# Performance work log

Measured on AMD Instinct MI355X. Metric: run time of the kernel, lower is better.

Reference implementation:

```python
import jax, jax.numpy as jnp
import numpy as np

MODES = 16
DIM = 16      # comb(modes + photons - 1, photons) with photons=1 -> modes
BATCH = 32768


def _mesh_targets(modes):
    # Full rectangular Clements mesh, 0-indexed mode pairs, modes*(modes-1)/2 elements.
    pairs = []
    for layer in range(modes):
        for i in range(layer % 2, modes - 1, 2):
            pairs.append((i, i + 1))
    return np.asarray(pairs, dtype=np.int32)


def setup_inputs() -> dict:
    key = jax.random.key(0)
    k1, k2, k3 = jax.random.split(key, 3)
    targets = jnp.asarray(_mesh_targets(MODES))  # [120, 2] int32
    E = targets.shape[0]
    params = jax.random.normal(k1, (BATCH, 2 * E), dtype=jnp.float32)
    state_re = jax.random.normal(k2, (BATCH, DIM, DIM), dtype=jnp.float32)
    state_im = jax.random.normal(k3, (BATCH, DIM, DIM), dtype=jnp.float32)
    return {"params": params, "state_re": state_re, "state_im": state_im, "targets": targets}


def _clements_unitary(theta, phi, m_idx, n_idx):
    # Sequentially embed 2x2 MZI blocks T(m,n,theta,phi) into a DIMxDIM unitary:
    # U <- T @ U, where T is identity except rows (m, n):
    #   T[m,m]=e^{i phi} cos th, T[m,n]=-sin th, T[n,m]=e^{i phi} sin th, T[n,n]=cos th
    # Only two rows of U change per step, so we update rows instead of a full matmul.
    U0 = jnp.eye(DIM, dtype=jnp.complex64)

    def step(U, x):
        mi, ni, t, p = x
        c = jnp.cos(t)
        s = jnp.sin(t)
        e = jnp.exp(1j * p)  # complex64
        rm = U[mi]
        rn = U[ni]
        U = U.at[mi].set(e * c * rm - s * rn)
        U = U.at[ni].set(e * s * rm + c * rn)
        return U, None

    U, _ = jax.lax.scan(step, U0, (m_idx, n_idx, theta, phi))
    # diag phases are all zero in UParamLayer.map_clements -> identity, skipped.
    return U


def reference(params, state_re, state_im, targets):
    E = targets.shape[0]
    theta = params[:, :E]          # [B, E]
    phi = params[:, E:2 * E]       # [B, E]
    m_idx = targets[:, 0]
    n_idx = targets[:, 1]

    U = jax.vmap(lambda t, p: _clements_unitary(t, p, m_idx, n_idx))(theta, phi)  # [B, D, D] c64
    rho = jax.lax.complex(state_re, state_im)  # [B, D, D] c64

    left = jnp.einsum('bij,bjk->bik', U, rho)             # U @ rho
    out = jnp.einsum('bik,bjk->bij', left, jnp.conj(U))   # (U @ rho) @ U^dagger
    # Return real/imag stacked so the baseline output is a plain float tensor.
    return jnp.stack([out.real, out.imag], axis=1)  # [B, 2, D, D] f32
```

## Files before the change

kernel.cpp:

```cpp
#include <hip/hip_runtime.h>

#define DIM 16
#define NE 120
#define ITEMS 8
#define THREADS 128
#define UITEM 1032
#define LDS_FLOATS (ITEMS * UITEM)

typedef float v2f __attribute__((ext_vector_type(2)));


__global__ __launch_bounds__(THREADS, 2) void uparam_kernel(
    const float* __restrict__ params,
    const float* __restrict__ state_re,
    const float* __restrict__ state_im,
    float* __restrict__ out)
{
    __shared__ float lds[LDS_FLOATS];

    const int tid  = threadIdx.x;
    const int item = tid >> 4;
    const int c    = tid & 15;
    const long b   = (long)blockIdx.x * ITEMS + item;

    float* slot = lds + item * UITEM;
    float* aux  = slot + 512;

    {
        const float* prow = params + b * (2 * NE);
        #pragma unroll
        for (int k = 0; k < 15; ++k) {
            const int a = k * 16 + c;
            float sv, cv;
            __sincosf(prow[a], &sv, &cv);
            const int e   = (a < NE) ? a : a - NE;
            const int off = (a < NE) ? 0 : 2;
            *(float2*)(aux + 4 * e + off) = make_float2(cv, sv);
        }
    }

    const float* rre = state_re + b * (DIM * DIM);
    const float* rim = state_im + b * (DIM * DIM);
    float prr[16], pri[16];
    #pragma unroll
    for (int k = 0; k < 16; ++k) { prr[k] = rre[k * 16 + c]; pri[k] = rim[k * 16 + c]; }

    asm volatile("s_waitcnt lgkmcnt(0)" ::: "memory");

    v2f Uv[DIM];
    #pragma unroll
    for (int i = 0; i < DIM; ++i) Uv[i] = (v2f){ (i == c) ? 1.0f : 0.0f, 0.0f };

    #pragma unroll 1
    for (int l2 = 0; l2 < 8; ++l2) {
        const int eb = l2 * 15;
        #pragma unroll
        for (int j = 0; j < 15; ++j) {
            const int m = (j < 8) ? 2 * j : 2 * (j - 8) + 1;
            const int n = m + 1;
            const float4 cs = *(const float4*)(aux + 4 * (eb + j));
            const float ct = cs.x, st = cs.y, cp = cs.z, sp = cs.w;
            const v2f um = Uv[m], un = Uv[n];
            const v2f jm = { -um.y, um.x };
            const v2f w  = cp * um + sp * jm;
            Uv[m] = ct * w - st * un;
            Uv[n] = st * w + ct * un;
        }
    }

    #pragma unroll
    for (int q = 0; q < 8; ++q) {
        const int qq = q ^ (c & 7);
        *(float4*)(slot + c * 32 + qq * 4) =
            make_float4(Uv[2*q].x, Uv[2*q].y, Uv[2*q+1].x, Uv[2*q+1].y);
    }

    asm volatile("s_waitcnt lgkmcnt(0)" ::: "memory");

    v2f L[DIM];
    #pragma unroll
    for (int i = 0; i < DIM; ++i) L[i] = (v2f)(0.0f);

    #pragma unroll
    for (int k = 0; k < 16; ++k) {
        const float* ucol = slot + k * 32;
        const int kx = k & 7;
        const float4 q0 = *(const float4*)(ucol + (0 ^ kx) * 4);
        const float4 q1 = *(const float4*)(ucol + (1 ^ kx) * 4);
        const float4 q2 = *(const float4*)(ucol + (2 ^ kx) * 4);
        const float4 q3 = *(const float4*)(ucol + (3 ^ kx) * 4);
        const float4 q4 = *(const float4*)(ucol + (4 ^ kx) * 4);
        const float4 q5 = *(const float4*)(ucol + (5 ^ kx) * 4);
        const float4 q6 = *(const float4*)(ucol + (6 ^ kx) * 4);
        const float4 q7 = *(const float4*)(ucol + (7 ^ kx) * 4);
        const float pr = prr[k], pi = pri[k];
        v2f u[16];
        u[0]=(v2f){q0.x,q0.y}; u[1]=(v2f){q0.z,q0.w}; u[2]=(v2f){q1.x,q1.y}; u[3]=(v2f){q1.z,q1.w};
        u[4]=(v2f){q2.x,q2.y}; u[5]=(v2f){q2.z,q2.w}; u[6]=(v2f){q3.x,q3.y}; u[7]=(v2f){q3.z,q3.w};
        u[8]=(v2f){q4.x,q4.y}; u[9]=(v2f){q4.z,q4.w}; u[10]=(v2f){q5.x,q5.y}; u[11]=(v2f){q5.z,q5.w};
        u[12]=(v2f){q6.x,q6.y}; u[13]=(v2f){q6.z,q6.w}; u[14]=(v2f){q7.x,q7.y}; u[15]=(v2f){q7.z,q7.w};
        #pragma unroll
        for (int i = 0; i < 16; ++i) {
            L[i] += u[i] * pr;
            L[i] += (v2f){ -u[i].y, u[i].x } * pi;
        }
    }

    #pragma unroll
    for (int i = 0; i < 16; ++i)
        *(v2f*)(aux + i * 32 + 2 * (c ^ i)) = L[i];

    asm volatile("s_waitcnt lgkmcnt(0)" ::: "memory");

    v2f acc[DIM];
    #pragma unroll
    for (int j = 0; j < DIM; ++j) acc[j] = (v2f)(0.0f);

    #pragma unroll 4
    for (int k = 0; k < 16; ++k) {
        const v2f lk = *(const v2f*)(aux + c * 32 + 2 * (k ^ c));
        const float* ucol = slot + k * 32;
        const int kx = k & 7;
        const float4 q0 = *(const float4*)(ucol + (0 ^ kx) * 4);
        const float4 q1 = *(const float4*)(ucol + (1 ^ kx) * 4);
        const float4 q2 = *(const float4*)(ucol + (2 ^ kx) * 4);
        const float4 q3 = *(const float4*)(ucol + (3 ^ kx) * 4);
        const float4 q4 = *(const float4*)(ucol + (4 ^ kx) * 4);
        const float4 q5 = *(const float4*)(ucol + (5 ^ kx) * 4);
        const float4 q6 = *(const float4*)(ucol + (6 ^ kx) * 4);
        const float4 q7 = *(const float4*)(ucol + (7 ^ kx) * 4);
        v2f u[16];
        u[0]=(v2f){q0.x,q0.y}; u[1]=(v2f){q0.z,q0.w}; u[2]=(v2f){q1.x,q1.y}; u[3]=(v2f){q1.z,q1.w};
        u[4]=(v2f){q2.x,q2.y}; u[5]=(v2f){q2.z,q2.w}; u[6]=(v2f){q3.x,q3.y}; u[7]=(v2f){q3.z,q3.w};
        u[8]=(v2f){q4.x,q4.y}; u[9]=(v2f){q4.z,q4.w}; u[10]=(v2f){q5.x,q5.y}; u[11]=(v2f){q5.z,q5.w};
        u[12]=(v2f){q6.x,q6.y}; u[13]=(v2f){q6.z,q6.w}; u[14]=(v2f){q7.x,q7.y}; u[15]=(v2f){q7.z,q7.w};
        const float lr = lk.x, li = lk.y;
        #pragma unroll
        for (int j = 0; j < 16; ++j) {
            acc[j] += u[j] * lr;
            acc[j] += (v2f){ u[j].y, -u[j].x } * li;
        }
    }

    float* outp = out + b * (2 * DIM * DIM) + c * DIM;
    #pragma unroll
    for (int q = 0; q < 4; ++q) {
        *(float4*)(outp + 4 * q) =
            make_float4(acc[4*q].x, acc[4*q+1].x, acc[4*q+2].x, acc[4*q+3].x);
        *(float4*)(outp + DIM * DIM + 4 * q) =
            make_float4(-acc[4*q].y, -acc[4*q+1].y, -acc[4*q+2].y, -acc[4*q+3].y);
    }
}

extern "C" void kernel_launch(void* const* d_in, const int* in_sizes, int n_in,
                              void* d_out, int out_size, void* d_ws, size_t ws_size,
                              hipStream_t stream) {
    const float* params   = (const float*)d_in[0];
    const float* state_re = (const float*)d_in[1];
    const float* state_im = (const float*)d_in[2];
    float* out = (float*)d_out;

    const int batch = in_sizes[0] / (2 * NE);
    dim3 grid(batch / ITEMS);
    uparam_kernel<<<grid, THREADS, 0, stream>>>(params, state_re, state_im, out);
}
```

Baseline: 69.87 us.

## Shrink blocks to one wave, stage angles in two halves, transpose via shuffles

The block shrinks from two waves and 8 batch items to one wave and 4 items. The angle table in LDS is halved by computing sincos and building the MZI update for 60 elements at a time in two passes, with the raw angles held in registers. The LDS round trip that transposed L is replaced by a butterfly of __shfl_xor exchanges. Together these cut LDS per item and LDS traffic, which should raise occupancy. The costs are extra shuffle instructions, and L[k] is indexed inside a loop that is only unrolled by 4, so the compiler may spill L to scratch.

```diff
diff --git a/kernel.cpp b/kernel.cpp
--- a/kernel.cpp
+++ b/kernel.cpp
@@ -2,9 +2,9 @@
 
 #define DIM 16
 #define NE 120
-#define ITEMS 8
-#define THREADS 128
-#define UITEM 1032
+#define ITEMS 4
+#define THREADS 64
+#define UITEM 760
 #define LDS_FLOATS (ITEMS * UITEM)
 
 typedef float v2f __attribute__((ext_vector_type(2)));
@@ -26,46 +26,57 @@
     float* slot = lds + item * UITEM;
     float* aux  = slot + 512;
 
-    {
-        const float* prow = params + b * (2 * NE);
-        #pragma unroll
-        for (int k = 0; k < 15; ++k) {
-            const int a = k * 16 + c;
-            float sv, cv;
-            __sincosf(prow[a], &sv, &cv);
-            const int e   = (a < NE) ? a : a - NE;
-            const int off = (a < NE) ? 0 : 2;
-            *(float2*)(aux + 4 * e + off) = make_float2(cv, sv);
-        }
+    const float* prow = params + b * (2 * NE);
+    float ang0[8], ang1[8];
+    #pragma unroll
+    for (int k = 0; k < 8; ++k) {
+        const int a  = k * 16 + c;
+        const int aa = (a < 120) ? a : 119;
+        ang0[k] = prow[(aa < 60) ? aa : 60 + aa];
+        ang1[k] = prow[(aa < 60) ? 60 + aa : 120 + aa];
     }
-
     const float* rre = state_re + b * (DIM * DIM);
     const float* rim = state_im + b * (DIM * DIM);
     float prr[16], pri[16];
     #pragma unroll
     for (int k = 0; k < 16; ++k) { prr[k] = rre[k * 16 + c]; pri[k] = rim[k * 16 + c]; }
 
-    asm volatile("s_waitcnt lgkmcnt(0)" ::: "memory");
-
     v2f Uv[DIM];
     #pragma unroll
     for (int i = 0; i < DIM; ++i) Uv[i] = (v2f){ (i == c) ? 1.0f : 0.0f, 0.0f };
 
     #pragma unroll 1
-    for (int l2 = 0; l2 < 8; ++l2) {
-        const int eb = l2 * 15;
+    for (int bat = 0; bat < 2; ++bat) {
         #pragma unroll
-        for (int j = 0; j < 15; ++j) {
-            const int m = (j < 8) ? 2 * j : 2 * (j - 8) + 1;
-            const int n = m + 1;
-            const float4 cs = *(const float4*)(aux + 4 * (eb + j));
-            const float ct = cs.x, st = cs.y, cp = cs.z, sp = cs.w;
-            const v2f um = Uv[m], un = Uv[n];
-            const v2f jm = { -um.y, um.x };
-            const v2f w  = cp * um + sp * jm;
-            Uv[m] = ct * w - st * un;
-            Uv[n] = st * w + ct * un;
+        for (int k = 0; k < 8; ++k) {
+            const int a = k * 16 + c;
+            float sv, cv;
+            __sincosf(bat ? ang1[k] : ang0[k], &sv, &cv);
+            if (a < 120) {
+                const int el  = (a < 60) ? a : a - 60;
+                const int off = (a < 60) ? 0 : 2;
+                *(float2*)(aux + 4 * el + off) = make_float2(cv, sv);
+            }
         }
+        asm volatile("s_waitcnt lgkmcnt(0)" ::: "memory");
+
+        #pragma unroll 1
+        for (int l2 = 0; l2 < 4; ++l2) {
+            const int ebl = l2 * 15 + (bat ? 0 : 0);
+            #pragma unroll
+            for (int j = 0; j < 15; ++j) {
+                const int m = (j < 8) ? 2 * j : 2 * (j - 8) + 1;
+                const int n = m + 1;
+                const float4 cs = *(const float4*)(aux + 4 * (ebl + j));
+                const float ct = cs.x, st = cs.y, cp = cs.z, sp = cs.w;
+                const v2f um = Uv[m], un = Uv[n];
+                const v2f jm = { -um.y, um.x };
+                const v2f w  = cp * um + sp * jm;
+                Uv[m] = ct * w - st * un;
+                Uv[n] = st * w + ct * un;
+            }
+        }
+        asm volatile("s_waitcnt lgkmcnt(0)" ::: "memory");
     }
 
     #pragma unroll
@@ -74,7 +85,6 @@
         *(float4*)(slot + c * 32 + qq * 4) =
             make_float4(Uv[2*q].x, Uv[2*q].y, Uv[2*q+1].x, Uv[2*q+1].y);
     }
-
     asm volatile("s_waitcnt lgkmcnt(0)" ::: "memory");
 
     v2f L[DIM];
@@ -107,10 +117,23 @@
     }
 
     #pragma unroll
-    for (int i = 0; i < 16; ++i)
-        *(v2f*)(aux + i * 32 + 2 * (c ^ i)) = L[i];
-
-    asm volatile("s_waitcnt lgkmcnt(0)" ::: "memory");
+    for (int s = 1; s < 16; s <<= 1) {
+        const bool hi = (c & s) != 0;
+        #pragma unroll
+        for (int i = 0; i < 16; i += 2 * s) {
+            #pragma unroll
+            for (int t = 0; t < s; ++t) {
+                const int lo = i + t, jj = i + t + s;
+                const v2f a = L[lo], bb = L[jj];
+                v2f send, recv;
+                send = hi ? a : bb;
+                recv.x = __shfl_xor(send.x, s, 64);
+                recv.y = __shfl_xor(send.y, s, 64);
+                L[lo] = hi ? recv : a;
+                L[jj] = hi ? bb : recv;
+            }
+        }
+    }
 
     v2f acc[DIM];
     #pragma unroll
@@ -118,7 +141,6 @@
 
     #pragma unroll 4
     for (int k = 0; k < 16; ++k) {
-        const v2f lk = *(const v2f*)(aux + c * 32 + 2 * (k ^ c));
         const float* ucol = slot + k * 32;
         const int kx = k & 7;
         const float4 q0 = *(const float4*)(ucol + (0 ^ kx) * 4);
@@ -134,7 +156,7 @@
         u[4]=(v2f){q2.x,q2.y}; u[5]=(v2f){q2.z,q2.w}; u[6]=(v2f){q3.x,q3.y}; u[7]=(v2f){q3.z,q3.w};
         u[8]=(v2f){q4.x,q4.y}; u[9]=(v2f){q4.z,q4.w}; u[10]=(v2f){q5.x,q5.y}; u[11]=(v2f){q5.z,q5.w};
         u[12]=(v2f){q6.x,q6.y}; u[13]=(v2f){q6.z,q6.w}; u[14]=(v2f){q7.x,q7.y}; u[15]=(v2f){q7.z,q7.w};
-        const float lr = lk.x, li = lk.y;
+        const float lr = L[k].x, li = L[k].y;
         #pragma unroll
         for (int j = 0; j < 16; ++j) {
             acc[j] += u[j] * lr;
```

Result: slower. 72.14 us (+3.2%).
